# Kernel optimization log

Measured on AMD Instinct MI355X. Metric: run time of the kernel, lower is better.

Reference implementation:

```python
import math
import jax, jax.numpy as jnp
import numpy as np

HIDDEN = 2048
NUM_HEADS = 32
HEAD_DIM = HIDDEN // NUM_HEADS
NUM_BLOCKS = 4
INTER = 2 * HIDDEN
EPS = 1e-5
ROPE_THETA = 10000.0


def setup_inputs() -> dict:
    key = jax.random.key(0)
    ks = jax.random.split(key, 6)
    B, S = 2, 2048
    sc = 0.02
    return {
        "x": jax.random.normal(ks[0], (B, S, HIDDEN), jnp.float32),
        "attn_norm_w": jnp.ones((HIDDEN,), jnp.float32),
        "ffn_norm_w": jnp.ones((HIDDEN,), jnp.float32),
        "w_qkv": jax.random.normal(ks[1], (3 * HIDDEN, HIDDEN), jnp.float32) * sc,
        "w_o": jax.random.normal(ks[2], (HIDDEN, HIDDEN), jnp.float32) * sc,
        "w_up": jax.random.normal(ks[3], (2 * INTER, HIDDEN), jnp.float32) * sc,
        "w_down": jax.random.normal(ks[4], (HIDDEN, INTER), jnp.float32) * sc,
    }


def _rmsnorm(x, w):
    var = jnp.mean(x * x, axis=-1, keepdims=True)
    return x * jax.lax.rsqrt(var + EPS) * w


def _rope_cache(seq_len, dim, theta, scale):
    inv_freq = 1.0 / (theta ** (jnp.arange(0, dim, 2, dtype=jnp.float32) / dim))
    t = jnp.arange(seq_len, dtype=jnp.float32) / scale
    freqs = jnp.outer(t, inv_freq)                     # [S, D/2]
    emb = jnp.concatenate([freqs, freqs], axis=-1)     # [S, D]
    return jnp.cos(emb), jnp.sin(emb)


def _apply_rope(x, cos, sin):
    # x: [B, H, S, D]
    d2 = x.shape[-1] // 2
    x1, x2 = x[..., :d2], x[..., d2:]
    rot = jnp.concatenate([-x2, x1], axis=-1)
    return x * cos[None, None] + rot * sin[None, None]


def reference(x, attn_norm_w, ffn_norm_w, w_qkv, w_o, w_up, w_down):
    B, S, _ = x.shape
    residual = x
    h = _rmsnorm(x, attn_norm_w)

    qkv = jnp.einsum('bsh,oh->bso', h, w_qkv)
    qkv = qkv.reshape(B, S, 3, NUM_HEADS, HEAD_DIM)
    q, k, v = qkv[:, :, 0], qkv[:, :, 1], qkv[:, :, 2]
    q = q.transpose(0, 2, 1, 3)  # [B,H,S,D]
    k = k.transpose(0, 2, 1, 3)
    v = v.transpose(0, 2, 1, 3)

    cos, sin = _rope_cache(S, HEAD_DIM, ROPE_THETA, 1.0)
    q = _apply_rope(q, cos, sin)
    k = _apply_rope(k, cos, sin)

    scale = 1.0 / math.sqrt(HEAD_DIM)
    attn = jnp.einsum('bhqd,bhkd->bhqk', q, k) * scale

    num_blocks = max(1, min(NUM_BLOCKS, S))
    blk = math.ceil(S / num_blocks)
    pos = jnp.arange(S)
    block_ids = pos // blk
    block_mask = block_ids[:, None] != block_ids[None, :]
    causal_mask = pos[:, None] < pos[None, :]
    invalid = causal_mask | block_mask                 # [S,S]
    mask_floor = jnp.finfo(attn.dtype).min
    attn = jnp.where(invalid[None, None], mask_floor, attn)

    attn = jax.nn.softmax(attn, axis=-1)
    context = jnp.einsum('bhqk,bhkd->bhqd', attn, v)
    context = context.transpose(0, 2, 1, 3).reshape(B, S, HIDDEN)

    x = residual + jnp.einsum('bsh,oh->bso', context, w_o)

    residual = x
    h = _rmsnorm(x, ffn_norm_w)
    up = jnp.einsum('bsh,oh->bso', h, w_up)
    gate, value = up[..., :INTER], up[..., INTER:]
    down = jnp.einsum('bsi,oi->bso', jax.nn.silu(gate) * value, w_down)
    return residual + down
```

## Files before the change

### kernel.cpp

```cpp
#include <hip/hip_runtime.h>
#include <cstdint>
#include <cstddef>

typedef __bf16 bf16x8 __attribute__((ext_vector_type(8)));
typedef __bf16 bf16x4 __attribute__((ext_vector_type(4)));
typedef float  f32x4  __attribute__((ext_vector_type(4)));

#define TOKENS  4096
#define SEQLEN  2048
#define HID     2048
#define QKV_W   6144
#define UP_W    8192
#define INTER_  4096

__device__ __forceinline__ void async16(const void* g, void* l) {
  __builtin_amdgcn_global_load_lds(
      (__attribute__((address_space(1))) void*)(g),
      (__attribute__((address_space(3))) void*)(l), 16, 0, 0);
}

__global__ __launch_bounds__(256) void cvt_kernel(const float* __restrict__ src,
                                                  __bf16* __restrict__ dst, int n4) {
  int i = blockIdx.x * 256 + threadIdx.x;
  if (i >= n4) return;
  float4 f = ((const float4*)src)[i];
  bf16x4 o;
  o[0] = (__bf16)f.x; o[1] = (__bf16)f.y; o[2] = (__bf16)f.z; o[3] = (__bf16)f.w;
  ((bf16x4*)dst)[i] = o;
}

__global__ __launch_bounds__(256) void rmsnorm_kernel(const float* __restrict__ x,
                                                      const float* __restrict__ wgt,
                                                      __bf16* __restrict__ out) {
  const int tok = blockIdx.x;
  const int t = threadIdx.x;
  const float4* xr = (const float4*)(x + (long)tok * HID);
  float4 a = xr[t], b = xr[t + 256];
  float ss = a.x*a.x + a.y*a.y + a.z*a.z + a.w*a.w
           + b.x*b.x + b.y*b.y + b.z*b.z + b.w*b.w;
  #pragma unroll
  for (int off = 32; off; off >>= 1) ss += __shfl_xor(ss, off);
  __shared__ float red[4];
  if ((t & 63) == 0) red[t >> 6] = ss;
  __syncthreads();
  float tot = red[0] + red[1] + red[2] + red[3];
  float r = rsqrtf(tot * (1.0f / HID) + 1e-5f);
  const float4* wr = (const float4*)wgt;
  float4 wa = wr[t], wb = wr[t + 256];
  bf16x4 o0, o1;
  o0[0] = (__bf16)(a.x * r * wa.x); o0[1] = (__bf16)(a.y * r * wa.y);
  o0[2] = (__bf16)(a.z * r * wa.z); o0[3] = (__bf16)(a.w * r * wa.w);
  o1[0] = (__bf16)(b.x * r * wb.x); o1[1] = (__bf16)(b.y * r * wb.y);
  o1[2] = (__bf16)(b.z * r * wb.z); o1[3] = (__bf16)(b.w * r * wb.w);
  bf16x4* orow = (bf16x4*)(out + (long)tok * HID);
  orow[t] = o0; orow[t + 256] = o1;
}

template<bool OUT_BF16, bool ADD_RES, bool ROPE, bool SILU>
__global__ __launch_bounds__(256) void gemm_bt(const __bf16* __restrict__ A, int lda,
                                               const __bf16* __restrict__ B, int ldb,
                                               void* Cv, int ldc,
                                               const float* __restrict__ Res, int K) {
  __shared__ __align__(16) __bf16 As[128 * 64];
  __shared__ __align__(16) __bf16 Bs[128 * 64];
  const int t = threadIdx.x;
  const int lane = t & 63;
  const int w = t >> 6;
  const int wm = (w >> 1) * 64, wn = (w & 1) * 64;
  const int m0 = blockIdx.y * 128;
  const int n0 = SILU ? blockIdx.x * 64 : blockIdx.x * 128;
  const int sr = t >> 3;
  const int sc = (((t & 7) ^ (sr & 7)) * 8);
  const __bf16* Ag = A + (long)(m0 + sr) * lda + sc;
  const __bf16* Bg = B + (long)(n0 + sr) * ldb + sc;
  char* lA = (char*)As + t * 16;
  char* lB = (char*)Bs + t * 16;
  const int lr = lane & 15;
  const int lq = lane >> 4;
  f32x4 acc[4][4] = {};
  for (int k0 = 0; k0 < K; k0 += 64) {
    __syncthreads();
    #pragma unroll
    for (int c = 0; c < 4; c++)
      async16(Ag + (long)(c * 32) * lda + k0, lA + c * 4096);
    #pragma unroll
    for (int c = 0; c < 4; c++) {
      const long rowoff = SILU ? (long)((c & 1) * INTER_ + (c >> 1) * 32) * ldb
                               : (long)(c * 32) * ldb;
      async16(Bg + rowoff + k0, lB + c * 4096);
    }
    __syncthreads();
    #pragma unroll
    for (int ks = 0; ks < 2; ks++) {
      const int pos = (((ks * 4 + lq) ^ (lr & 7)) * 8);
      bf16x8 af[4], bfr[4];
      #pragma unroll
      for (int i = 0; i < 4; i++)
        af[i]  = *(const bf16x8*)(As + (wm + i * 16 + lr) * 64 + pos);
      #pragma unroll
      for (int j = 0; j < 4; j++)
        bfr[j] = *(const bf16x8*)(Bs + (wn + j * 16 + lr) * 64 + pos);
      #pragma unroll
      for (int i = 0; i < 4; i++)
        #pragma unroll
        for (int j = 0; j < 4; j++)
          acc[i][j] = __builtin_amdgcn_mfma_f32_16x16x32_bf16(af[i], bfr[j], acc[i][j], 0, 0, 0);
    }
  }
  const int lq4 = lq * 4;
  #pragma unroll
  for (int i = 0; i < 4; i++) {
    #pragma unroll
    for (int r = 0; r < 4; r++) {
      const long row = m0 + wm + i * 16 + lq4 + r;
      #pragma unroll
      for (int j = 0; j < 4; j++) {
        const long col = n0 + wn + j * 16 + lr;
        float v = acc[i][j][r];
        if (ADD_RES) v += Res[row * (long)ldc + col];
        if (OUT_BF16) ((__bf16*)Cv)[row * (long)ldc + col] = (__bf16)v;
        else          ((float*)Cv)[row * (long)ldc + col] = v;
      }
    }
  }
}

template<bool ROPE, bool SILU>
__global__ __launch_bounds__(512, 2) void gemm8p(const __bf16* __restrict__ A, int lda,
                                                 const __bf16* __restrict__ B, int ldb,
                                                 void* Cv, int ldc, int K) {
  __shared__ __align__(16) __bf16 As[2 * 16384];
  __shared__ __align__(16) __bf16 Bs[2 * 16384];
  const int tid  = threadIdx.x;
  const int lane = tid & 63;
  const int w    = tid >> 6;
  const int wm2  = w >> 2;
  const int wn4  = w & 3;
  const int lr   = lane & 15;
  const int lq   = lane >> 4;
  const int m0   = blockIdx.y * 256;
  const int n0   = ROPE ? blockIdx.x * 256 : 0;
  const int n0c  = SILU ? blockIdx.x * 128 : 0;

  const long r0 = tid >> 3;
  const int  e  = (((tid & 7) ^ ((int)r0 & 7)) * 8);
  const __bf16* Ap0 = A + (long)(m0 + r0) * lda + e;
  long br0, br1, bhs;
  if (ROPE) {
    br0 = n0 + 64 * (((int)r0 >> 5) & 3) + ((int)r0 & 31);
    br1 = n0 + 64 * ((((int)r0 + 64) >> 5) & 3) + ((int)r0 & 31);
    bhs = 32 * (long)ldb;
  } else {
    br0 = n0c + r0;
    br1 = n0c + r0 + 64;
    bhs = (long)INTER_ * ldb;
  }
  const __bf16* Bp0 = B + br0 * ldb + e;
  const __bf16* Bp1 = B + br1 * ldb + e;
  char* sA = (char*)As;
  char* sB = (char*)Bs;
  const int tid16 = tid * 16;

#define STAGE_A(h_, nb_, kk_) do {                                                     \
    async16(Ap0 + (long)((h_) * 128) * lda + (kk_),      sA + (nb_)*32768 + (h_)*16384 + tid16);        \
    async16(Ap0 + (long)((h_) * 128 + 64) * lda + (kk_), sA + (nb_)*32768 + (h_)*16384 + 8192 + tid16); \
  } while (0)
#define STAGE_B(h_, nb_, kk_) do {                                                     \
    async16(Bp0 + (h_) * bhs + (kk_), sB + (nb_)*32768 + (h_)*16384 + tid16);          \
    async16(Bp1 + (h_) * bhs + (kk_), sB + (nb_)*32768 + (h_)*16384 + 8192 + tid16);   \
  } while (0)

  const int ch0 = ((lq ^ (lr & 7)) * 16);
  const int ch1 = (((4 + lq) ^ (lr & 7)) * 16);
  const int abase = (wm2 * 64 + lr) * 128;
  const int bbase = (wn4 * 32 + lr) * 128;

  f32x4 acc[8][4] = {};
  bf16x8 af[4][2], bfr[4][2];
  const int NT = K >> 6;

#define LOAD_A(mh_) do {                                                               \
    _Pragma("unroll")                                                                  \
    for (int i = 0; i < 4; i++) {                                                      \
      af[i][0] = *(const bf16x8*)(Ab + abase + (mh_)*16384 + i*2048 + ch0);            \
      af[i][1] = *(const bf16x8*)(Ab + abase + (mh_)*16384 + i*2048 + ch1);            \
    } } while (0)
#define LOAD_B(nh_) do {                                                               \
    _Pragma("unroll")                                                                  \
    for (int j = 0; j < 2; j++) {                                                      \
      bfr[(nh_)*2 + j][0] = *(const bf16x8*)(Bb + bbase + (nh_)*16384 + j*2048 + ch0); \
      bfr[(nh_)*2 + j][1] = *(const bf16x8*)(Bb + bbase + (nh_)*16384 + j*2048 + ch1); \
    } } while (0)
#define MFMA_Q(mh_, nh_) do {                                                          \
    __builtin_amdgcn_s_setprio(1);                                                     \
    _Pragma("unroll")                                                                  \
    for (int ks = 0; ks < 2; ks++)                                                     \
      _Pragma("unroll")                                                                \
      for (int i = 0; i < 4; i++)                                                      \
        _Pragma("unroll")                                                              \
        for (int j = 0; j < 2; j++)                                                    \
          acc[(mh_)*4 + i][(nh_)*2 + j] = __builtin_amdgcn_mfma_f32_16x16x32_bf16(     \
              af[i][ks], bfr[(nh_)*2 + j][ks], acc[(mh_)*4 + i][(nh_)*2 + j], 0, 0, 0);\
    __builtin_amdgcn_s_setprio(0);                                                     \
  } while (0)
#define SBAR() do { __builtin_amdgcn_sched_barrier(0);                                 \
    __builtin_amdgcn_s_barrier(); __builtin_amdgcn_sched_barrier(0); } while (0)
#define LGKM0() do { asm volatile("s_waitcnt lgkmcnt(0)" ::: "memory");                \
    __builtin_amdgcn_sched_barrier(0); } while (0)

  STAGE_A(0, 0, 0); STAGE_B(0, 0, 0); STAGE_B(1, 0, 0); STAGE_A(1, 0, 0);
  asm volatile("s_waitcnt vmcnt(4)" ::: "memory");
  SBAR();

  for (int T = 0; T < NT; ++T) {
    const int cb = T & 1, nb = cb ^ 1;
    const int kk = (T + 1) << 6;
    const bool st = (T + 1 < NT);
    const char* Ab = (const char*)As + cb * 32768;
    const char* Bb = (const char*)Bs + cb * 32768;
    LOAD_A(0); LOAD_B(0);
    if (st) { STAGE_A(0, nb, kk); STAGE_B(0, nb, kk); }
    SBAR(); LGKM0();
    MFMA_Q(0, 0);
    if (st) asm volatile("s_waitcnt vmcnt(6)" ::: "memory");
    else    asm volatile("s_waitcnt vmcnt(2)" ::: "memory");
    SBAR();
    LOAD_B(1);
    if (st) STAGE_B(1, nb, kk);
    SBAR(); LGKM0();
    MFMA_Q(0, 1);
    if (st) asm volatile("s_waitcnt vmcnt(6)" ::: "memory");
    else    asm volatile("s_waitcnt vmcnt(0)" ::: "memory");
    SBAR();
    LOAD_A(1);
    if (st) STAGE_A(1, nb, kk);
    SBAR(); LGKM0();
    MFMA_Q(1, 0);
    SBAR();
    MFMA_Q(1, 1);
    if (st) asm volatile("s_waitcnt vmcnt(4)" ::: "memory");
    SBAR();
  }
#undef STAGE_A
#undef STAGE_B
#undef LOAD_A
#undef LOAD_B
#undef MFMA_Q
#undef SBAR
#undef LGKM0

  const int lq4 = lq * 4;
  if (ROPE) {
    if (n0 < 4096) {
      const float invf0 = exp2f((float)(lr)      * -0.41524101186092029f);
      const float invf1 = exp2f((float)(16 + lr) * -0.41524101186092029f);
      #pragma unroll
      for (int mi = 0; mi < 8; mi++) {
        #pragma unroll
        for (int r = 0; r < 4; r++) {
          const long row = m0 + (mi >> 2) * 128 + wm2 * 64 + (mi & 3) * 16 + lq4 + r;
          const float s = (float)(int)(row & (SEQLEN - 1));
          __bf16* crow = (__bf16*)Cv + row * (long)ldc + n0 + wn4 * 64 + lr;
          #pragma unroll
          for (int nj = 0; nj < 2; nj++) {
            float x1 = acc[mi][nj][r], x2 = acc[mi][nj + 2][r];
            float ang = s * (nj ? invf1 : invf0);
            float sn, cs;
            __sincosf(ang, &sn, &cs);
            crow[nj * 16]      = (__bf16)(x1 * cs - x2 * sn);
            crow[nj * 16 + 32] = (__bf16)(x2 * cs + x1 * sn);
          }
        }
      }
    } else {
      #pragma unroll
      for (int mi = 0; mi < 8; mi++) {
        #pragma unroll
        for (int r = 0; r < 4; r++) {
          const long row = m0 + (mi >> 2) * 128 + wm2 * 64 + (mi & 3) * 16 + lq4 + r;
          __bf16* crow = (__bf16*)Cv + row * (long)ldc + n0 + wn4 * 64 + lr;
          #pragma unroll
          for (int njf = 0; njf < 4; njf++)
            crow[(njf >> 1) * 32 + (njf & 1) * 16] = (__bf16)acc[mi][njf][r];
        }
      }
    }
  } else {
    #pragma unroll
    for (int mi = 0; mi < 8; mi++) {
      #pragma unroll
      for (int r = 0; r < 4; r++) {
        const long row = m0 + (mi >> 2) * 128 + wm2 * 64 + (mi & 3) * 16 + lq4 + r;
        #pragma unroll
        for (int nj = 0; nj < 2; nj++) {
          const long col = n0c + wn4 * 32 + nj * 16 + lr;
          float g = acc[mi][nj][r];
          float v = acc[mi][nj + 2][r];
          float sg = g / (1.0f + __expf(-g));
          ((__bf16*)Cv)[row * (long)ldc + col] = (__bf16)(sg * v);
        }
      }
    }
  }
}

#define VTS 520
__global__ __launch_bounds__(256) void attn_kernel(const __bf16* __restrict__ qkv,
                                                   __bf16* __restrict__ ctx) {
  const int qt = blockIdx.x;
  const int h  = blockIdx.y;
  const int b  = blockIdx.z;
  const int w    = threadIdx.x >> 6;
  const int lane = threadIdx.x & 63;
  const int lr = lane & 15;
  const int lq = lane >> 4;
  const int q0   = qt * 64;
  const int blk0 = (q0 >> 9) << 9;
  const int nkv  = q0 + 64 - blk0;
  const long tok0 = (long)b * SEQLEN;

  const int qrow = q0 + w * 16 + lr;
  const long qoff = (tok0 + qrow) * QKV_W + h * 64 + lq * 8;
  bf16x8 qf0 = *(const bf16x8*)(qkv + qoff);
  bf16x8 qf1 = *(const bf16x8*)(qkv + qoff + 32);

  __shared__ __align__(16) __bf16 VT[64][VTS];
  __shared__ __align__(16) __bf16 Pb[4][16][48];

  {
    const int vc = (threadIdx.x & 7) * 8;
    for (int kv = threadIdx.x >> 3; kv < nkv; kv += 32) {
      bf16x8 v8 = *(const bf16x8*)(qkv + (tok0 + blk0 + kv) * QKV_W + 2 * HID + h * 64 + vc);
      #pragma unroll
      for (int i = 0; i < 8; i++) VT[vc + i][kv] = v8[i];
    }
  }
  __syncthreads();

  float m[4], l[4];
  f32x4 oacc[4] = {};
  #pragma unroll
  for (int r = 0; r < 4; r++) { m[r] = -1e30f; l[r] = 0.0f; }

  const int myrow = q0 + w * 16 + lq * 4;

  for (int kv0 = 0; kv0 < nkv; kv0 += 32) {
    f32x4 s[2];
    #pragma unroll
    for (int nt = 0; nt < 2; nt++) {
      const long koff = (tok0 + blk0 + kv0 + nt * 16 + lr) * QKV_W + HID + h * 64 + lq * 8;
      bf16x8 kf0 = *(const bf16x8*)(qkv + koff);
      bf16x8 kf1 = *(const bf16x8*)(qkv + koff + 32);
      f32x4 sa = {0.0f, 0.0f, 0.0f, 0.0f};
      sa = __builtin_amdgcn_mfma_f32_16x16x32_bf16(qf0, kf0, sa, 0, 0, 0);
      sa = __builtin_amdgcn_mfma_f32_16x16x32_bf16(qf1, kf1, sa, 0, 0, 0);
      const int kpos = blk0 + kv0 + nt * 16 + lr;
      #pragma unroll
      for (int r = 0; r < 4; r++) {
        float v = sa[r] * 0.125f;
        s[nt][r] = (kpos <= myrow + r) ? v : -1e30f;
      }
    }
    float p0[4], p1[4], alpha[4];
    #pragma unroll
    for (int r = 0; r < 4; r++) {
      float mx = fmaxf(s[0][r], s[1][r]);
      mx = fmaxf(mx, __shfl_xor(mx, 1));
      mx = fmaxf(mx, __shfl_xor(mx, 2));
      mx = fmaxf(mx, __shfl_xor(mx, 4));
      mx = fmaxf(mx, __shfl_xor(mx, 8));
      float mn = fmaxf(m[r], mx);
      alpha[r] = __expf(m[r] - mn);
      m[r] = mn;
      p0[r] = __expf(s[0][r] - mn);
      p1[r] = __expf(s[1][r] - mn);
      float rs = p0[r] + p1[r];
      rs += __shfl_xor(rs, 1);
      rs += __shfl_xor(rs, 2);
      rs += __shfl_xor(rs, 4);
      rs += __shfl_xor(rs, 8);
      l[r] = l[r] * alpha[r] + rs;
    }
    #pragma unroll
    for (int dt = 0; dt < 4; dt++)
      #pragma unroll
      for (int r = 0; r < 4; r++) oacc[dt][r] *= alpha[r];

    #pragma unroll
    for (int r = 0; r < 4; r++) {
      Pb[w][lq * 4 + r][lr]      = (__bf16)p0[r];
      Pb[w][lq * 4 + r][16 + lr] = (__bf16)p1[r];
    }
    asm volatile("s_waitcnt lgkmcnt(0)" ::: "memory");
    bf16x8 pf = *(const bf16x8*)(&Pb[w][lr][lq * 8]);
    #pragma unroll
    for (int dt = 0; dt < 4; dt++) {
      bf16x8 vf = *(const bf16x8*)(&VT[dt * 16 + lr][kv0 + lq * 8]);
      oacc[dt] = __builtin_amdgcn_mfma_f32_16x16x32_bf16(pf, vf, oacc[dt], 0, 0, 0);
    }
  }
  #pragma unroll
  for (int r = 0; r < 4; r++) {
    float inv = 1.0f / l[r];
    long obase = (tok0 + myrow + r) * HID + h * 64;
    #pragma unroll
    for (int dt = 0; dt < 4; dt++)
      ctx[obase + dt * 16 + lr] = (__bf16)(oacc[dt][r] * inv);
  }
}

extern "C" void kernel_launch(void* const* d_in, const int* in_sizes, int n_in,
                              void* d_out, int out_size, void* d_ws, size_t ws_size,
                              hipStream_t stream) {
  const float* x      = (const float*)d_in[0];
  const float* anw    = (const float*)d_in[1];
  const float* fnw    = (const float*)d_in[2];
  const float* w_qkv  = (const float*)d_in[3];
  const float* w_o    = (const float*)d_in[4];
  const float* w_up   = (const float*)d_in[5];
  const float* w_down = (const float*)d_in[6];
  float* out = (float*)d_out;

  char* wsb = (char*)d_ws;
  __bf16* ABUF = (__bf16*)wsb;
  __bf16* QKV  = (__bf16*)(wsb + (size_t)16777216);
  __bf16* WBUF = (__bf16*)(wsb + (size_t)83886080);
  __bf16* ACT  = QKV;

  rmsnorm_kernel<<<TOKENS, 256, 0, stream>>>(x, anw, ABUF);
  cvt_kernel<<<(QKV_W * HID / 4 + 255) / 256, 256, 0, stream>>>(w_qkv, WBUF, QKV_W * HID / 4);
  gemm8p<true, false><<<dim3(QKV_W / 256, TOKENS / 256), 512, 0, stream>>>(
      ABUF, HID, WBUF, HID, (void*)QKV, QKV_W, HID);
  attn_kernel<<<dim3(SEQLEN / 64, 32, 2), 256, 0, stream>>>(QKV, ABUF);
  cvt_kernel<<<(HID * HID / 4 + 255) / 256, 256, 0, stream>>>(w_o, WBUF, HID * HID / 4);
  gemm_bt<false, true, false, false><<<dim3(HID / 128, TOKENS / 128), 256, 0, stream>>>(
      ABUF, HID, WBUF, HID, (void*)out, HID, x, HID);

  rmsnorm_kernel<<<TOKENS, 256, 0, stream>>>(out, fnw, ABUF);
  cvt_kernel<<<(UP_W * HID / 4 + 255) / 256, 256, 0, stream>>>(w_up, WBUF, UP_W * HID / 4);
  gemm8p<false, true><<<dim3(INTER_ / 128, TOKENS / 256), 512, 0, stream>>>(
      ABUF, HID, WBUF, HID, (void*)ACT, INTER_, HID);
  cvt_kernel<<<(HID * INTER_ / 4 + 255) / 256, 256, 0, stream>>>(w_down, WBUF, HID * INTER_ / 4);
  gemm_bt<false, true, false, false><<<dim3(HID / 128, TOKENS / 128), 256, 0, stream>>>(
      ACT, INTER_, WBUF, INTER_, (void*)out, HID, out, INTER_);
}
```

Baseline: 589.3 us.

## Pipeline K/V loads in attention with double-buffered swizzled LDS tiles

The attention kernel no longer stages the whole V block transposed into a large LDS array before the loop. It now streams one 32-row V tile at a time into a small double-buffered, XOR-swizzled LDS region and prefetches the next K fragments into registers while the current tile is computed. The goal is less LDS per block and more overlap of global loads with MFMA and softmax work, and the swizzle is meant to cut bank conflicts on the transposed V and P stores. In exchange it adds two block-wide barriers per 32-key step, which can stall the waves.

```diff
diff --git a/kernel.cpp b/kernel.cpp
--- a/kernel.cpp
+++ b/kernel.cpp
@@ -304,36 +304,55 @@
   }
 }
 
-#define VTS 520
 __global__ __launch_bounds__(256) void attn_kernel(const __bf16* __restrict__ qkv,
                                                    __bf16* __restrict__ ctx) {
-  const int qt = blockIdx.x;
-  const int h  = blockIdx.y;
-  const int b  = blockIdx.z;
+  const int qt   = blockIdx.x;
+  const int head = blockIdx.y;
+  const int b    = blockIdx.z;
   const int w    = threadIdx.x >> 6;
   const int lane = threadIdx.x & 63;
   const int lr = lane & 15;
   const int lq = lane >> 4;
   const int q0   = qt * 64;
-  const int blk0 = (q0 >> 9) << 9;
+  const int blk0 = q0 & ~511;
   const int nkv  = q0 + 64 - blk0;
+  const int NT   = nkv >> 5;
   const long tok0 = (long)b * SEQLEN;
 
   const int qrow = q0 + w * 16 + lr;
-  const long qoff = (tok0 + qrow) * QKV_W + h * 64 + lq * 8;
+  const long qoff = (tok0 + qrow) * QKV_W + head * 64 + lq * 8;
   bf16x8 qf0 = *(const bf16x8*)(qkv + qoff);
   bf16x8 qf1 = *(const bf16x8*)(qkv + qoff + 32);
 
-  __shared__ __align__(16) __bf16 VT[64][VTS];
-  __shared__ __align__(16) __bf16 Pb[4][16][48];
-
+  __shared__ __align__(16) char VTb[8192];
+  __shared__ __align__(16) char Pbb[8192];
+
+  const __bf16* kp = qkv + (tok0 + blk0 + lr) * QKV_W + HID + head * 64 + lq * 8;
+  const int skv = threadIdx.x & 31;
+  const int sd0 = (threadIdx.x >> 5) * 8;
+  const __bf16* vp = qkv + (tok0 + blk0 + skv) * QKV_W + 2 * HID + head * 64 + sd0;
+
+  bf16x8 ka[2][2], kb[2][2];
+
+#define LOADK(KN, tk) do { \
+    KN[0][0] = *(const bf16x8*)(kp + (long)(tk) * QKV_W); \
+    KN[0][1] = *(const bf16x8*)(kp + (long)(tk) * QKV_W + 32); \
+    KN[1][0] = *(const bf16x8*)(kp + (long)((tk) + 16) * QKV_W); \
+    KN[1][1] = *(const bf16x8*)(kp + (long)((tk) + 16) * QKV_W + 32); \
+  } while (0)
+
+#define WRITEV(vr_, hb_) do { \
+    const int c_ = (hb_) * 4 + (skv >> 3); \
+    char* vb_ = VTb + sd0 * 128 + ((skv & 7) * 2); \
+    _Pragma("unroll") \
+    for (int i_ = 0; i_ < 8; i_++) \
+      *(__bf16*)(vb_ + i_ * 128 + ((c_ ^ i_) * 16)) = vr_[i_]; \
+  } while (0)
+
+  LOADK(ka, 0);
   {
-    const int vc = (threadIdx.x & 7) * 8;
-    for (int kv = threadIdx.x >> 3; kv < nkv; kv += 32) {
-      bf16x8 v8 = *(const bf16x8*)(qkv + (tok0 + blk0 + kv) * QKV_W + 2 * HID + h * 64 + vc);
-      #pragma unroll
-      for (int i = 0; i < 8; i++) VT[vc + i][kv] = v8[i];
-    }
+    bf16x8 vr0 = *(const bf16x8*)(vp);
+    WRITEV(vr0, 0);
   }
   __syncthreads();
 
@@ -341,68 +360,79 @@
   f32x4 oacc[4] = {};
   #pragma unroll
   for (int r = 0; r < 4; r++) { m[r] = -1e30f; l[r] = 0.0f; }
-
   const int myrow = q0 + w * 16 + lq * 4;
 
-  for (int kv0 = 0; kv0 < nkv; kv0 += 32) {
-    f32x4 s[2];
-    #pragma unroll
-    for (int nt = 0; nt < 2; nt++) {
-      const long koff = (tok0 + blk0 + kv0 + nt * 16 + lr) * QKV_W + HID + h * 64 + lq * 8;
-      bf16x8 kf0 = *(const bf16x8*)(qkv + koff);
-      bf16x8 kf1 = *(const bf16x8*)(qkv + koff + 32);
-      f32x4 sa = {0.0f, 0.0f, 0.0f, 0.0f};
-      sa = __builtin_amdgcn_mfma_f32_16x16x32_bf16(qf0, kf0, sa, 0, 0, 0);
-      sa = __builtin_amdgcn_mfma_f32_16x16x32_bf16(qf1, kf1, sa, 0, 0, 0);
-      const int kpos = blk0 + kv0 + nt * 16 + lr;
-      #pragma unroll
-      for (int r = 0; r < 4; r++) {
-        float v = sa[r] * 0.125f;
-        s[nt][r] = (kpos <= myrow + r) ? v : -1e30f;
-      }
-    }
-    float p0[4], p1[4], alpha[4];
-    #pragma unroll
-    for (int r = 0; r < 4; r++) {
-      float mx = fmaxf(s[0][r], s[1][r]);
-      mx = fmaxf(mx, __shfl_xor(mx, 1));
-      mx = fmaxf(mx, __shfl_xor(mx, 2));
-      mx = fmaxf(mx, __shfl_xor(mx, 4));
-      mx = fmaxf(mx, __shfl_xor(mx, 8));
-      float mn = fmaxf(m[r], mx);
-      alpha[r] = __expf(m[r] - mn);
-      m[r] = mn;
-      p0[r] = __expf(s[0][r] - mn);
-      p1[r] = __expf(s[1][r] - mn);
-      float rs = p0[r] + p1[r];
-      rs += __shfl_xor(rs, 1);
-      rs += __shfl_xor(rs, 2);
-      rs += __shfl_xor(rs, 4);
-      rs += __shfl_xor(rs, 8);
-      l[r] = l[r] * alpha[r] + rs;
-    }
-    #pragma unroll
-    for (int dt = 0; dt < 4; dt++)
-      #pragma unroll
-      for (int r = 0; r < 4; r++) oacc[dt][r] *= alpha[r];
-
-    #pragma unroll
-    for (int r = 0; r < 4; r++) {
-      Pb[w][lq * 4 + r][lr]      = (__bf16)p0[r];
-      Pb[w][lq * 4 + r][16 + lr] = (__bf16)p1[r];
-    }
-    asm volatile("s_waitcnt lgkmcnt(0)" ::: "memory");
-    bf16x8 pf = *(const bf16x8*)(&Pb[w][lr][lq * 8]);
-    #pragma unroll
-    for (int dt = 0; dt < 4; dt++) {
-      bf16x8 vf = *(const bf16x8*)(&VT[dt * 16 + lr][kv0 + lq * 8]);
-      oacc[dt] = __builtin_amdgcn_mfma_f32_16x16x32_bf16(pf, vf, oacc[dt], 0, 0, 0);
-    }
-  }
+#define ITER(t_, hb_, KC, KN) { \
+    const int tkn_ = ((t_) + 1) * 32; \
+    const bool more_ = ((t_) + 1 < NT); \
+    bf16x8 vr_ = {}; \
+    if (more_) { LOADK(KN, tkn_); vr_ = *(const bf16x8*)(vp + (long)tkn_ * QKV_W); } \
+    f32x4 s0 = {0.f, 0.f, 0.f, 0.f}, s1 = {0.f, 0.f, 0.f, 0.f}; \
+    s0 = __builtin_amdgcn_mfma_f32_16x16x32_bf16(qf0, KC[0][0], s0, 0, 0, 0); \
+    s0 = __builtin_amdgcn_mfma_f32_16x16x32_bf16(qf1, KC[0][1], s0, 0, 0, 0); \
+    s1 = __builtin_amdgcn_mfma_f32_16x16x32_bf16(qf0, KC[1][0], s1, 0, 0, 0); \
+    s1 = __builtin_amdgcn_mfma_f32_16x16x32_bf16(qf1, KC[1][1], s1, 0, 0, 0); \
+    const int kpos0_ = blk0 + (t_) * 32 + lr; \
+    float p0[4], p1[4], alpha[4]; \
+    _Pragma("unroll") \
+    for (int r = 0; r < 4; r++) { \
+      float v0 = s0[r] * 0.125f, v1 = s1[r] * 0.125f; \
+      v0 = (kpos0_      <= myrow + r) ? v0 : -1e30f; \
+      v1 = (kpos0_ + 16 <= myrow + r) ? v1 : -1e30f; \
+      float mx = fmaxf(v0, v1); \
+      mx = fmaxf(mx, __shfl_xor(mx, 1)); \
+      mx = fmaxf(mx, __shfl_xor(mx, 2)); \
+      mx = fmaxf(mx, __shfl_xor(mx, 4)); \
+      mx = fmaxf(mx, __shfl_xor(mx, 8)); \
+      float mn = fmaxf(m[r], mx); \
+      alpha[r] = __expf(m[r] - mn); \
+      m[r] = mn; \
+      p0[r] = __expf(v0 - mn); \
+      p1[r] = __expf(v1 - mn); \
+      float rs = p0[r] + p1[r]; \
+      rs += __shfl_xor(rs, 1); rs += __shfl_xor(rs, 2); \
+      rs += __shfl_xor(rs, 4); rs += __shfl_xor(rs, 8); \
+      l[r] = l[r] * alpha[r] + rs; \
+    } \
+    _Pragma("unroll") \
+    for (int dt = 0; dt < 4; dt++) \
+      _Pragma("unroll") \
+      for (int r = 0; r < 4; r++) oacc[dt][r] *= alpha[r]; \
+    { \
+      char* pw_ = Pbb + w * 2048 + (lq * 4) * 128 + ((lr & 7) * 2); \
+      const int cl_ = (hb_) * 4 + (lr >> 3); \
+      _Pragma("unroll") \
+      for (int r = 0; r < 4; r++) { \
+        const int q7_ = (lq * 4 + r) & 7; \
+        *(__bf16*)(pw_ + r * 128 + (((cl_    ) ^ q7_) * 16)) = (__bf16)p0[r]; \
+        *(__bf16*)(pw_ + r * 128 + (((cl_ + 2) ^ q7_) * 16)) = (__bf16)p1[r]; \
+      } \
+    } \
+    asm volatile("s_waitcnt lgkmcnt(0)" ::: "memory"); \
+    const int swz_ = (((hb_) * 4 + lq) ^ (lr & 7)) * 16; \
+    bf16x8 pf_ = *(const bf16x8*)(Pbb + w * 2048 + lr * 128 + swz_); \
+    _Pragma("unroll") \
+    for (int dt = 0; dt < 4; dt++) { \
+      bf16x8 vf_ = *(const bf16x8*)(VTb + dt * 2048 + lr * 128 + swz_); \
+      oacc[dt] = __builtin_amdgcn_mfma_f32_16x16x32_bf16(pf_, vf_, oacc[dt], 0, 0, 0); \
+    } \
+    __syncthreads(); \
+    if (more_) WRITEV(vr_, (hb_) ^ 1); \
+    __syncthreads(); \
+  }
+
+  for (int t2 = 0; t2 < NT; t2 += 2) {
+    ITER(t2, 0, ka, kb)
+    ITER(t2 + 1, 1, kb, ka)
+  }
+#undef ITER
+#undef LOADK
+#undef WRITEV
+
   #pragma unroll
   for (int r = 0; r < 4; r++) {
     float inv = 1.0f / l[r];
-    long obase = (tok0 + myrow + r) * HID + h * 64;
+    long obase = (tok0 + myrow + r) * HID + head * 64;
     #pragma unroll
     for (int dt = 0; dt < 4; dt++)
       ctx[obase + dt * 16 + lr] = (__bf16)(oacc[dt][r] * inv);
```

New measurement: 566.2 us. 3.9% less time.

## Stream V tiles with double-buffered swizzled LDS and split QKV GEMM

Applied to the files above, without the earlier changes.

The attention kernel now streams V in 64-key tiles through a double-buffered, XOR-swizzled LDS buffer. This replaces the up-front transposed load of the whole causal block, cutting LDS footprint and bank conflicts and letting the next V load overlap compute. Each iteration handles 64 keys instead of 32, and the P scratch is swizzled too. The QKV GEMM is split into a 256-wide gemm8p for the Q/K columns and a 128-tile gemm_bt for the V columns, which adds a launch and a barrier per tile in exchange for better occupancy.

```diff
diff --git a/kernel.cpp b/kernel.cpp
--- a/kernel.cpp
+++ b/kernel.cpp
@@ -304,36 +304,47 @@
   }
 }
 
-#define VTS 520
 __global__ __launch_bounds__(256) void attn_kernel(const __bf16* __restrict__ qkv,
                                                    __bf16* __restrict__ ctx) {
-  const int qt = blockIdx.x;
-  const int h  = blockIdx.y;
-  const int b  = blockIdx.z;
+  const int qt   = blockIdx.x;
+  const int head = blockIdx.y;
+  const int b    = blockIdx.z;
   const int w    = threadIdx.x >> 6;
   const int lane = threadIdx.x & 63;
   const int lr = lane & 15;
   const int lq = lane >> 4;
   const int q0   = qt * 64;
-  const int blk0 = (q0 >> 9) << 9;
+  const int blk0 = q0 & ~511;
   const int nkv  = q0 + 64 - blk0;
+  const int NT   = nkv >> 6;
   const long tok0 = (long)b * SEQLEN;
 
   const int qrow = q0 + w * 16 + lr;
-  const long qoff = (tok0 + qrow) * QKV_W + h * 64 + lq * 8;
+  const long qoff = (tok0 + qrow) * QKV_W + head * 64 + lq * 8;
   bf16x8 qf0 = *(const bf16x8*)(qkv + qoff);
   bf16x8 qf1 = *(const bf16x8*)(qkv + qoff + 32);
 
-  __shared__ __align__(16) __bf16 VT[64][VTS];
-  __shared__ __align__(16) __bf16 Pb[4][16][48];
+  __shared__ __align__(16) char VTb[2][8192];
+  __shared__ __align__(16) char Pbb[8192];
+
+  const int skv = threadIdx.x & 63;
+  const int sd0 = (threadIdx.x >> 6) * 8;
+  const __bf16* vp = qkv + (tok0 + blk0 + skv) * QKV_W + 2 * HID + head * 64 + sd0;
+  const __bf16* kp = qkv + (tok0 + blk0 + lr) * QKV_W + HID + head * 64 + lq * 8;
+
+#define WRITEV(va_, vb_, bf_) do { \
+    const int c_ = skv >> 3; \
+    char* p_ = VTb[bf_] + sd0 * 128 + ((skv & 7) * 2); \
+    _Pragma("unroll") \
+    for (int i_ = 0; i_ < 8; i_++) { \
+      *(__bf16*)(p_ + i_ * 128 + ((c_ ^ i_) * 16))        = va_[i_]; \
+      *(__bf16*)(p_ + (32 + i_) * 128 + ((c_ ^ i_) * 16)) = vb_[i_]; \
+    } } while (0)
 
   {
-    const int vc = (threadIdx.x & 7) * 8;
-    for (int kv = threadIdx.x >> 3; kv < nkv; kv += 32) {
-      bf16x8 v8 = *(const bf16x8*)(qkv + (tok0 + blk0 + kv) * QKV_W + 2 * HID + h * 64 + vc);
-      #pragma unroll
-      for (int i = 0; i < 8; i++) VT[vc + i][kv] = v8[i];
-    }
+    bf16x8 va0 = *(const bf16x8*)(vp);
+    bf16x8 vb0 = *(const bf16x8*)(vp + 32);
+    WRITEV(va0, vb0, 0);
   }
   __syncthreads();
 
@@ -341,30 +352,41 @@
   f32x4 oacc[4] = {};
   #pragma unroll
   for (int r = 0; r < 4; r++) { m[r] = -1e30f; l[r] = 0.0f; }
-
   const int myrow = q0 + w * 16 + lq * 4;
 
-  for (int kv0 = 0; kv0 < nkv; kv0 += 32) {
-    f32x4 s[2];
-    #pragma unroll
-    for (int nt = 0; nt < 2; nt++) {
-      const long koff = (tok0 + blk0 + kv0 + nt * 16 + lr) * QKV_W + HID + h * 64 + lq * 8;
-      bf16x8 kf0 = *(const bf16x8*)(qkv + koff);
-      bf16x8 kf1 = *(const bf16x8*)(qkv + koff + 32);
-      f32x4 sa = {0.0f, 0.0f, 0.0f, 0.0f};
-      sa = __builtin_amdgcn_mfma_f32_16x16x32_bf16(qf0, kf0, sa, 0, 0, 0);
-      sa = __builtin_amdgcn_mfma_f32_16x16x32_bf16(qf1, kf1, sa, 0, 0, 0);
-      const int kpos = blk0 + kv0 + nt * 16 + lr;
-      #pragma unroll
-      for (int r = 0; r < 4; r++) {
-        float v = sa[r] * 0.125f;
-        s[nt][r] = (kpos <= myrow + r) ? v : -1e30f;
-      }
-    }
-    float p0[4], p1[4], alpha[4];
+  for (int t = 0; t < NT; ++t) {
+    const int bf = t & 1;
+    const bool more = (t + 1 < NT);
+    bf16x8 va = {}, vb = {};
+    if (more) {
+      const __bf16* vq = vp + (long)((t + 1) * 64) * QKV_W;
+      va = *(const bf16x8*)(vq);
+      vb = *(const bf16x8*)(vq + 32);
+    }
+    const __bf16* kpt = kp + (long)(t * 64) * QKV_W;
+    bf16x8 kf[4][2];
+    #pragma unroll
+    for (int nt = 0; nt < 4; nt++) {
+      kf[nt][0] = *(const bf16x8*)(kpt + (long)(nt * 16) * QKV_W);
+      kf[nt][1] = *(const bf16x8*)(kpt + (long)(nt * 16) * QKV_W + 32);
+    }
+    f32x4 s[4];
+    #pragma unroll
+    for (int nt = 0; nt < 4; nt++) {
+      f32x4 z = {0.f, 0.f, 0.f, 0.f};
+      z = __builtin_amdgcn_mfma_f32_16x16x32_bf16(qf0, kf[nt][0], z, 0, 0, 0);
+      z = __builtin_amdgcn_mfma_f32_16x16x32_bf16(qf1, kf[nt][1], z, 0, 0, 0);
+      s[nt] = z;
+    }
+    const int kb0 = blk0 + t * 64 + lr;
+    float p[4][4], alpha[4];
     #pragma unroll
     for (int r = 0; r < 4; r++) {
-      float mx = fmaxf(s[0][r], s[1][r]);
+      float v0 = (kb0      <= myrow + r) ? s[0][r] * 0.125f : -1e30f;
+      float v1 = (kb0 + 16 <= myrow + r) ? s[1][r] * 0.125f : -1e30f;
+      float v2 = (kb0 + 32 <= myrow + r) ? s[2][r] * 0.125f : -1e30f;
+      float v3 = (kb0 + 48 <= myrow + r) ? s[3][r] * 0.125f : -1e30f;
+      float mx = fmaxf(fmaxf(v0, v1), fmaxf(v2, v3));
       mx = fmaxf(mx, __shfl_xor(mx, 1));
       mx = fmaxf(mx, __shfl_xor(mx, 2));
       mx = fmaxf(mx, __shfl_xor(mx, 4));
@@ -372,9 +394,11 @@
       float mn = fmaxf(m[r], mx);
       alpha[r] = __expf(m[r] - mn);
       m[r] = mn;
-      p0[r] = __expf(s[0][r] - mn);
-      p1[r] = __expf(s[1][r] - mn);
-      float rs = p0[r] + p1[r];
+      p[0][r] = __expf(v0 - mn);
+      p[1][r] = __expf(v1 - mn);
+      p[2][r] = __expf(v2 - mn);
+      p[3][r] = __expf(v3 - mn);
+      float rs = (p[0][r] + p[1][r]) + (p[2][r] + p[3][r]);
       rs += __shfl_xor(rs, 1);
       rs += __shfl_xor(rs, 2);
       rs += __shfl_xor(rs, 4);
@@ -385,24 +409,39 @@
     for (int dt = 0; dt < 4; dt++)
       #pragma unroll
       for (int r = 0; r < 4; r++) oacc[dt][r] *= alpha[r];
-
-    #pragma unroll
-    for (int r = 0; r < 4; r++) {
-      Pb[w][lq * 4 + r][lr]      = (__bf16)p0[r];
-      Pb[w][lq * 4 + r][16 + lr] = (__bf16)p1[r];
+    {
+      char* pw = Pbb + w * 2048 + (lq * 4) * 128 + ((lr & 7) * 2);
+      const int cb_ = lr >> 3;
+      #pragma unroll
+      for (int r = 0; r < 4; r++) {
+        const int q7 = (lq * 4 + r) & 7;
+        #pragma unroll
+        for (int nt = 0; nt < 4; nt++)
+          *(__bf16*)(pw + r * 128 + (((nt * 2 + cb_) ^ q7) * 16)) = (__bf16)p[nt][r];
+      }
     }
     asm volatile("s_waitcnt lgkmcnt(0)" ::: "memory");
-    bf16x8 pf = *(const bf16x8*)(&Pb[w][lr][lq * 8]);
-    #pragma unroll
-    for (int dt = 0; dt < 4; dt++) {
-      bf16x8 vf = *(const bf16x8*)(&VT[dt * 16 + lr][kv0 + lq * 8]);
-      oacc[dt] = __builtin_amdgcn_mfma_f32_16x16x32_bf16(pf, vf, oacc[dt], 0, 0, 0);
-    }
-  }
+    #pragma unroll
+    for (int h = 0; h < 2; h++) {
+      const int swz = (((h * 4 + lq) ^ (lr & 7)) * 16);
+      bf16x8 pf = *(const bf16x8*)(Pbb + w * 2048 + lr * 128 + swz);
+      #pragma unroll
+      for (int dt = 0; dt < 4; dt++) {
+        bf16x8 vf = *(const bf16x8*)(VTb[bf] + (dt * 16 + lr) * 128 + swz);
+        oacc[dt] = __builtin_amdgcn_mfma_f32_16x16x32_bf16(pf, vf, oacc[dt], 0, 0, 0);
+      }
+    }
+    if (more) {
+      WRITEV(va, vb, bf ^ 1);
+      __syncthreads();
+    }
+  }
+#undef WRITEV
+
   #pragma unroll
   for (int r = 0; r < 4; r++) {
     float inv = 1.0f / l[r];
-    long obase = (tok0 + myrow + r) * HID + h * 64;
+    long obase = (tok0 + myrow + r) * HID + head * 64;
     #pragma unroll
     for (int dt = 0; dt < 4; dt++)
       ctx[obase + dt * 16 + lr] = (__bf16)(oacc[dt][r] * inv);
@@ -429,8 +468,10 @@
 
   rmsnorm_kernel<<<TOKENS, 256, 0, stream>>>(x, anw, ABUF);
   cvt_kernel<<<(QKV_W * HID / 4 + 255) / 256, 256, 0, stream>>>(w_qkv, WBUF, QKV_W * HID / 4);
-  gemm8p<true, false><<<dim3(QKV_W / 256, TOKENS / 256), 512, 0, stream>>>(
+  gemm8p<true, false><<<dim3(4096 / 256, TOKENS / 256), 512, 0, stream>>>(
       ABUF, HID, WBUF, HID, (void*)QKV, QKV_W, HID);
+  gemm_bt<true, false, false, false><<<dim3(HID / 128, TOKENS / 128), 256, 0, stream>>>(
+      ABUF, HID, WBUF + (size_t)4096 * HID, HID, (void*)(QKV + 4096), QKV_W, nullptr, HID);
   attn_kernel<<<dim3(SEQLEN / 64, 32, 2), 256, 0, stream>>>(QKV, ABUF);
   cvt_kernel<<<(HID * HID / 4 + 255) / 256, 256, 0, stream>>>(w_o, WBUF, HID * HID / 4);
   gemm_bt<false, true, false, false><<<dim3(HID / 128, TOKENS / 128), 256, 0, stream>>>(
```

Result: faster. 554.6 us (-5.9%).
